# Optimization experiments

Hardware: AMD Instinct MI355X
Metric: run time of the kernel (lower is better)

## Reference

```python
import jax, jax.numpy as jnp
import numpy as np

X_DIM, Y_DIM, HIDDEN, N = 768, 768, 300, 768


def setup_inputs() -> dict:
    key = jax.random.key(0)
    ks = jax.random.split(key, 7)
    lim1 = 1.0 / np.sqrt(X_DIM + Y_DIM)
    lim2 = 1.0 / np.sqrt(HIDDEN)
    return {
        "x_samples": jax.random.normal(ks[0], (N, X_DIM), dtype=jnp.float32),
        "y_samples": jax.random.normal(ks[1], (N, Y_DIM), dtype=jnp.float32),
        "perm": jax.random.permutation(ks[2], N).astype(jnp.int32),
        # Linear 1: (x_dim+y_dim) -> hidden, torch default uniform init
        "W1": jax.random.uniform(ks[3], (HIDDEN, X_DIM + Y_DIM), jnp.float32, -lim1, lim1),
        "b1": jax.random.uniform(ks[4], (HIDDEN,), jnp.float32, -lim1, lim1),
        # Linear 2: hidden -> 1
        "W2": jax.random.uniform(ks[5], (1, HIDDEN), jnp.float32, -lim2, lim2),
        "b2": jax.random.uniform(ks[6], (1,), jnp.float32, -lim2, lim2),
    }


def reference(x_samples, y_samples, perm, W1, b1, W2, b2):
    n = x_samples.shape[0]
    x_dim = x_samples.shape[1]
    # First linear is separable across the concat: split W1 into x- and y-parts.
    hx = x_samples @ W1[:, :x_dim].T            # [N, H]
    hy = y_samples @ W1[:, x_dim:].T            # [N, H]
    w2 = W2[0]                                   # [H]
    # T0: matched pairs (x_i, y_i)
    t0 = jax.nn.softplus(jax.nn.relu(hx + hy + b1) @ w2 + b2[0])   # [N]
    # T1[i, j] = F(x_j, y_perm[i]) -- pairwise tile, [N, N, H] intermediate
    hyp = hy[perm]                               # [N, H]
    hpair = jax.nn.relu(hyp[:, None, :] + hx[None, :, :] + b1)     # [N, N, H]
    t1 = jax.nn.softplus(hpair @ w2 + b2[0])     # [N, N]
    lower_bound = t0.mean() - (jax.nn.logsumexp(t1, axis=1).mean() - jnp.log(n).astype(t1.dtype))
    return lower_bound
```

## Files before the change

kernel.cpp:

```cpp
#include <hip/hip_runtime.h>
#include <math.h>

#define NN   768
#define HH   300
#define HPAD 320
#define KD   768

#define P_OFF    0
#define PKS_STR  245760
#define PG_STR   1966080
#define CF_OFF   3932160
#define AF_OFF   4177920
#define SP_OFF   4423680
#define SP_STR   589824
#define ES_OFF   9142272
#define T0_OFF   9143040

__global__ __launch_bounds__(256) void k1_gemm(
    const float* __restrict__ x, const float* __restrict__ y,
    const int* __restrict__ perm, const float* __restrict__ W1,
    float* __restrict__ wsf)
{
    const int tid = threadIdx.x;
    const int tx = tid & 15;
    const int ty = tid >> 4;
    const int i0 = blockIdx.x * 128;
    const int h0 = blockIdx.y * 64;
    const int g  = blockIdx.z & 1;
    const int ks = blockIdx.z >> 1;
    const int kbeg = ks * 96;

    const float* src = g ? y : x;
    const int koff = g ? KD : 0;

    __shared__ float Xt[32][132];
    __shared__ float Wt[32][68];

    float4 acc[4][2];
    #pragma unroll
    for (int r = 0; r < 4; ++r) { acc[r][0] = make_float4(0,0,0,0);
                                  acc[r][1] = make_float4(0,0,0,0); }

    const int kq = (tid & 7) << 2;
    const float* xp[4];
    int xr[4];
    #pragma unroll
    for (int it = 0; it < 4; ++it) {
        int row = ((tid + it*256) >> 3);
        int gr = i0 + row;
        if (g) gr = perm[gr];
        xp[it] = src + (size_t)gr * KD + kbeg + kq;
        xr[it] = row;
    }
    const float* wp[2];
    int wr[2]; bool wv[2];
    #pragma unroll
    for (int it = 0; it < 2; ++it) {
        int hrow = ((tid + it*256) >> 3);
        int hg = h0 + hrow;
        wv[it] = hg < HH;
        wp[it] = W1 + (size_t)(wv[it] ? hg : 0) * (2*KD) + koff + kbeg + kq;
        wr[it] = hrow;
    }

    for (int kb = 0; kb < 96; kb += 32) {
        float4 xv[4], wvv[2];
        #pragma unroll
        for (int it = 0; it < 4; ++it) xv[it] = *(const float4*)(xp[it] + kb);
        #pragma unroll
        for (int it = 0; it < 2; ++it) {
            wvv[it] = *(const float4*)(wp[it] + kb);
            if (!wv[it]) wvv[it] = make_float4(0,0,0,0);
        }
        if (kb) __syncthreads();
        #pragma unroll
        for (int it = 0; it < 4; ++it) {
            Xt[kq+0][xr[it]] = xv[it].x; Xt[kq+1][xr[it]] = xv[it].y;
            Xt[kq+2][xr[it]] = xv[it].z; Xt[kq+3][xr[it]] = xv[it].w;
        }
        #pragma unroll
        for (int it = 0; it < 2; ++it) {
            Wt[kq+0][wr[it]] = wvv[it].x; Wt[kq+1][wr[it]] = wvv[it].y;
            Wt[kq+2][wr[it]] = wvv[it].z; Wt[kq+3][wr[it]] = wvv[it].w;
        }
        __syncthreads();

        #pragma unroll 8
        for (int k = 0; k < 32; ++k) {
            float4 a  = *(const float4*)&Wt[k][4*ty];
            float4 b0 = *(const float4*)&Xt[k][4*tx];
            float4 b1v = *(const float4*)&Xt[k][64 + 4*tx];
            float ar[4] = {a.x, a.y, a.z, a.w};
            #pragma unroll
            for (int r = 0; r < 4; ++r) {
                acc[r][0].x = fmaf(ar[r], b0.x,  acc[r][0].x);
                acc[r][0].y = fmaf(ar[r], b0.y,  acc[r][0].y);
                acc[r][0].z = fmaf(ar[r], b0.z,  acc[r][0].z);
                acc[r][0].w = fmaf(ar[r], b0.w,  acc[r][0].w);
                acc[r][1].x = fmaf(ar[r], b1v.x, acc[r][1].x);
                acc[r][1].y = fmaf(ar[r], b1v.y, acc[r][1].y);
                acc[r][1].z = fmaf(ar[r], b1v.z, acc[r][1].z);
                acc[r][1].w = fmaf(ar[r], b1v.w, acc[r][1].w);
            }
        }
    }

    float* dst = wsf + P_OFF + (size_t)(g*8 + ks) * PKS_STR;
    #pragma unroll
    for (int r = 0; r < 4; ++r) {
        float* rp = dst + (size_t)(h0 + 4*ty + r) * NN + i0;
        *(float4*)(rp + 4*tx)      = acc[r][0];
        *(float4*)(rp + 64 + 4*tx) = acc[r][1];
    }
}

__global__ __launch_bounds__(256) void k1b_combine(
    const float* __restrict__ b1, float* __restrict__ wsf)
{
    int idx = blockIdx.x * 256 + threadIdx.x;
    int g = idx >= 61440;
    int rem = idx - g * 61440;
    int h = rem / 192;
    int i4 = (rem % 192) * 4;

    float4 o = make_float4(0.f,0.f,0.f,0.f);
    if (h < HH) {
        const float* p = wsf + P_OFF + (size_t)g * PG_STR + (size_t)h * NN + i4;
        #pragma unroll
        for (int ks = 0; ks < 8; ++ks) {
            float4 v = *(const float4*)(p + (size_t)ks * PKS_STR);
            o.x += v.x; o.y += v.y; o.z += v.z; o.w += v.w;
        }
        if (g) {
            float bv = b1[h];
            o.x += bv; o.y += bv; o.z += bv; o.w += bv;
        }
    }
    float* dst = wsf + (g ? AF_OFF : CF_OFF) + (size_t)h * NN + i4;
    *(float4*)dst = o;
}

__global__ __launch_bounds__(256) void k2_pair(
    const float* __restrict__ wsf, const float* __restrict__ w2,
    float* __restrict__ sp)
{
    const int tid = threadIdx.x;
    const int tx = tid & 15;
    const int ty = tid >> 4;
    const int j0 = blockIdx.x * 128;
    const int i0 = blockIdx.y * 64;
    const int p  = blockIdx.z;
    const int h0 = p * 38;

    const float* AF = wsf + AF_OFF;
    const float* CF = wsf + CF_OFF;

    __shared__ float As[38][68];
    __shared__ float Cs[38][132];
    __shared__ float w2s[38];

    for (int e = tid; e < 608; e += 256) {
        int h = e >> 4, q = (e & 15) * 4;
        *(float4*)&As[h][q] = *(const float4*)(AF + (size_t)(h0 + h) * NN + i0 + q);
    }
    for (int e = tid; e < 1216; e += 256) {
        int h = e >> 5, q = (e & 31) * 4;
        *(float4*)&Cs[h][q] = *(const float4*)(CF + (size_t)(h0 + h) * NN + j0 + q);
    }
    if (tid < 38) {
        int h = h0 + tid;
        w2s[tid] = (h < HH) ? w2[h] : 0.f;
    }
    __syncthreads();

    float acc[4][8];
    #pragma unroll
    for (int r = 0; r < 4; ++r)
        #pragma unroll
        for (int c = 0; c < 8; ++c) acc[r][c] = 0.f;

    #pragma unroll 2
    for (int h = 0; h < 38; ++h) {
        float wh = w2s[h];
        float4 av = *(const float4*)&As[h][4*ty];
        float4 c0 = *(const float4*)&Cs[h][4*tx];
        float4 c1 = *(const float4*)&Cs[h][64 + 4*tx];
        float ar[4] = {av.x, av.y, av.z, av.w};
        float cr[8] = {c0.x, c0.y, c0.z, c0.w, c1.x, c1.y, c1.z, c1.w};
        #pragma unroll
        for (int r = 0; r < 4; ++r) {
            #pragma unroll
            for (int c = 0; c < 8; ++c) {
                float t = fmaxf(ar[r] + cr[c], 0.f);
                acc[r][c] = fmaf(t, wh, acc[r][c]);
            }
        }
    }

    float* dst = sp + (size_t)p * SP_STR;
    #pragma unroll
    for (int r = 0; r < 4; ++r) {
        float* rp = dst + (size_t)(i0 + 4*ty + r) * NN + j0;
        *(float4*)(rp + 4*tx) =
            make_float4(acc[r][0], acc[r][1], acc[r][2], acc[r][3]);
        *(float4*)(rp + 64 + 4*tx) =
            make_float4(acc[r][4], acc[r][5], acc[r][6], acc[r][7]);
    }
}

__global__ __launch_bounds__(256) void k2e_rows(
    const float* __restrict__ wsf, const int* __restrict__ perm,
    const float* __restrict__ b2,
    float* __restrict__ esum, float* __restrict__ t0c)
{
    const int tid = threadIdx.x;
    const float b2v = b2[0];
    const int row = blockIdx.x;
    const int pj = perm[row];
    const float* spr = wsf + SP_OFF + (size_t)row * NN;
    __shared__ float red[256];

    float e = 0.f;
    #pragma unroll
    for (int jj = 0; jj < 3; ++jj) {
        int j = tid + jj * 256;
        float s = 0.f;
        #pragma unroll
        for (int p = 0; p < 8; ++p) s += spr[(size_t)p * SP_STR + j];
        float u = s + b2v;
        e += expf(u);
        if (j == pj) {
            t0c[row] = (u > 0.f) ? u + log1pf(expf(-u)) : log1pf(expf(u));
        }
    }
    red[tid] = e;
    __syncthreads();
    for (int s = 128; s > 0; s >>= 1) {
        if (tid < s) red[tid] += red[tid + s];
        __syncthreads();
    }
    if (tid == 0) esum[row] = red[0];
}

__global__ __launch_bounds__(256) void k3_final(
    const float* __restrict__ wsf, float* __restrict__ out)
{
    const int tid = threadIdx.x;
    const float* esum = wsf + ES_OFF;
    const float* t0   = wsf + T0_OFF;

    double st0 = 0.0, slse = 0.0;
    for (int i = tid; i < NN; i += 256) {
        st0  += (double)t0[i];
        slse += log((double)NN + (double)esum[i]);
    }
    __shared__ double sa[256], sb[256];
    sa[tid] = st0; sb[tid] = slse;
    __syncthreads();
    for (int s = 128; s > 0; s >>= 1) {
        if (tid < s) { sa[tid] += sa[tid+s]; sb[tid] += sb[tid+s]; }
        __syncthreads();
    }
    if (tid == 0) {
        double lb = st0 = sa[0]/(double)NN - (sb[0]/(double)NN - log((double)NN));
        out[0] = (float)lb;
    }
}

extern "C" void kernel_launch(void* const* d_in, const int* in_sizes, int n_in,
                              void* d_out, int out_size, void* d_ws, size_t ws_size,
                              hipStream_t stream) {
    const float* x    = (const float*)d_in[0];
    const float* y    = (const float*)d_in[1];
    const int*   perm = (const int*)  d_in[2];
    const float* W1   = (const float*)d_in[3];
    const float* b1   = (const float*)d_in[4];
    const float* W2   = (const float*)d_in[5];
    const float* b2   = (const float*)d_in[6];
    float* wsf = (float*)d_ws;
    float* out = (float*)d_out;

    k1_gemm    <<<dim3(6,5,16),  256, 0, stream>>>(x, y, perm, W1, wsf);
    k1b_combine<<<480,           256, 0, stream>>>(b1, wsf);
    k2_pair    <<<dim3(6,12,8),  256, 0, stream>>>(wsf, W2, wsf + SP_OFF);
    k2e_rows   <<<NN,            256, 0, stream>>>(wsf, perm, b2,
                                                   wsf + ES_OFF, wsf + T0_OFF);
    k3_final   <<<1,             256, 0, stream>>>(wsf, out);
}
```

Baseline: 118.6 us.

## Retile pairwise kernel to 4 hidden splits and fuse final reduction via atomic counter

The pairwise relu-dot kernel is retiled to 48x96 output tiles with 75 hidden units per split and 4 splits instead of 8. This halves the partial-sum buffers written and then re-read by the row kernel, and drops the padded hidden tail. The final scalar reduction kernel is folded into the row kernel with a last-block-done atomic counter, which removes one launch. The cost is a 3x6 per-thread microtile, which does less register reuse per LDS read, plus some extra atomics and fences.

```diff
diff --git a/kernel.cpp b/kernel.cpp
--- a/kernel.cpp
+++ b/kernel.cpp
@@ -3,7 +3,6 @@
 
 #define NN   768
 #define HH   300
-#define HPAD 320
 #define KD   768
 
 #define P_OFF    0
@@ -15,6 +14,7 @@
 #define SP_STR   589824
 #define ES_OFF   9142272
 #define T0_OFF   9143040
+#define CNT_OFF  9143808
 
 __global__ __launch_bounds__(256) void k1_gemm(
     const float* __restrict__ x, const float* __restrict__ y,
@@ -118,6 +118,7 @@
     const float* __restrict__ b1, float* __restrict__ wsf)
 {
     int idx = blockIdx.x * 256 + threadIdx.x;
+    if (idx == 0) *(unsigned int*)(wsf + CNT_OFF) = 0u;
     int g = idx >= 61440;
     int rem = idx - g * 61440;
     int h = rem / 192;
@@ -147,50 +148,48 @@
     const int tid = threadIdx.x;
     const int tx = tid & 15;
     const int ty = tid >> 4;
-    const int j0 = blockIdx.x * 128;
-    const int i0 = blockIdx.y * 64;
+    const int j0 = blockIdx.x * 96;
+    const int i0 = blockIdx.y * 48;
     const int p  = blockIdx.z;
-    const int h0 = p * 38;
+    const int h0 = p * 75;
 
     const float* AF = wsf + AF_OFF;
     const float* CF = wsf + CF_OFF;
 
-    __shared__ float As[38][68];
-    __shared__ float Cs[38][132];
-    __shared__ float w2s[38];
-
-    for (int e = tid; e < 608; e += 256) {
-        int h = e >> 4, q = (e & 15) * 4;
+    __shared__ float As[75][52];
+    __shared__ float Cs[75][100];
+    __shared__ float w2s[75];
+
+    for (int e = tid; e < 900; e += 256) {
+        int h = e / 12, q = (e % 12) * 4;
         *(float4*)&As[h][q] = *(const float4*)(AF + (size_t)(h0 + h) * NN + i0 + q);
     }
-    for (int e = tid; e < 1216; e += 256) {
-        int h = e >> 5, q = (e & 31) * 4;
+    for (int e = tid; e < 1800; e += 256) {
+        int h = e / 24, q = (e % 24) * 4;
         *(float4*)&Cs[h][q] = *(const float4*)(CF + (size_t)(h0 + h) * NN + j0 + q);
     }
-    if (tid < 38) {
-        int h = h0 + tid;
-        w2s[tid] = (h < HH) ? w2[h] : 0.f;
-    }
+    if (tid < 75) w2s[tid] = w2[h0 + tid];
     __syncthreads();
 
-    float acc[4][8];
-    #pragma unroll
-    for (int r = 0; r < 4; ++r)
-        #pragma unroll
-        for (int c = 0; c < 8; ++c) acc[r][c] = 0.f;
-
-    #pragma unroll 2
-    for (int h = 0; h < 38; ++h) {
+    float acc[3][6];
+    #pragma unroll
+    for (int r = 0; r < 3; ++r)
+        #pragma unroll
+        for (int c = 0; c < 6; ++c) acc[r][c] = 0.f;
+
+    #pragma unroll 3
+    for (int h = 0; h < 75; ++h) {
         float wh = w2s[h];
-        float4 av = *(const float4*)&As[h][4*ty];
-        float4 c0 = *(const float4*)&Cs[h][4*tx];
-        float4 c1 = *(const float4*)&Cs[h][64 + 4*tx];
-        float ar[4] = {av.x, av.y, av.z, av.w};
-        float cr[8] = {c0.x, c0.y, c0.z, c0.w, c1.x, c1.y, c1.z, c1.w};
-        #pragma unroll
-        for (int r = 0; r < 4; ++r) {
+        float2 a01 = *(const float2*)&As[h][2*ty];
+        float  a2  = As[h][32 + ty];
+        float4 c03 = *(const float4*)&Cs[h][4*tx];
+        float2 c45 = *(const float2*)&Cs[h][64 + 2*tx];
+        float ar[3] = {a01.x, a01.y, a2};
+        float cr[6] = {c03.x, c03.y, c03.z, c03.w, c45.x, c45.y};
+        #pragma unroll
+        for (int r = 0; r < 3; ++r) {
             #pragma unroll
-            for (int c = 0; c < 8; ++c) {
+            for (int c = 0; c < 6; ++c) {
                 float t = fmaxf(ar[r] + cr[c], 0.f);
                 acc[r][c] = fmaf(t, wh, acc[r][c]);
             }
@@ -199,19 +198,20 @@
 
     float* dst = sp + (size_t)p * SP_STR;
     #pragma unroll
-    for (int r = 0; r < 4; ++r) {
-        float* rp = dst + (size_t)(i0 + 4*ty + r) * NN + j0;
+    for (int r = 0; r < 3; ++r) {
+        int i = (r < 2) ? (i0 + 2*ty + r) : (i0 + 32 + ty);
+        float* rp = dst + (size_t)i * NN + j0;
         *(float4*)(rp + 4*tx) =
             make_float4(acc[r][0], acc[r][1], acc[r][2], acc[r][3]);
-        *(float4*)(rp + 64 + 4*tx) =
-            make_float4(acc[r][4], acc[r][5], acc[r][6], acc[r][7]);
+        *(float2*)(rp + 64 + 2*tx) = make_float2(acc[r][4], acc[r][5]);
     }
 }
 
 __global__ __launch_bounds__(256) void k2e_rows(
     const float* __restrict__ wsf, const int* __restrict__ perm,
     const float* __restrict__ b2,
-    float* __restrict__ esum, float* __restrict__ t0c)
+    float* __restrict__ esum, float* __restrict__ t0c,
+    unsigned int* __restrict__ cnt, float* __restrict__ out)
 {
     const int tid = threadIdx.x;
     const float b2v = b2[0];
@@ -219,18 +219,21 @@
     const int pj = perm[row];
     const float* spr = wsf + SP_OFF + (size_t)row * NN;
     __shared__ float red[256];
+    __shared__ int last;
 
     float e = 0.f;
     #pragma unroll
     for (int jj = 0; jj < 3; ++jj) {
         int j = tid + jj * 256;
-        float s = 0.f;
-        #pragma unroll
-        for (int p = 0; p < 8; ++p) s += spr[(size_t)p * SP_STR + j];
+        float s = spr[j]
+                + spr[(size_t)1 * SP_STR + j]
+                + spr[(size_t)2 * SP_STR + j]
+                + spr[(size_t)3 * SP_STR + j];
         float u = s + b2v;
         e += expf(u);
         if (j == pj) {
-            t0c[row] = (u > 0.f) ? u + log1pf(expf(-u)) : log1pf(expf(u));
+            float t0 = (u > 0.f) ? u + log1pf(expf(-u)) : log1pf(expf(u));
+            atomicExch(&t0c[row], t0);
         }
     }
     red[tid] = e;
@@ -239,31 +242,34 @@
         if (tid < s) red[tid] += red[tid + s];
         __syncthreads();
     }
-    if (tid == 0) esum[row] = red[0];
-}
-
-__global__ __launch_bounds__(256) void k3_final(
-    const float* __restrict__ wsf, float* __restrict__ out)
-{
-    const int tid = threadIdx.x;
-    const float* esum = wsf + ES_OFF;
-    const float* t0   = wsf + T0_OFF;
-
-    double st0 = 0.0, slse = 0.0;
-    for (int i = tid; i < NN; i += 256) {
-        st0  += (double)t0[i];
-        slse += log((double)NN + (double)esum[i]);
-    }
-    __shared__ double sa[256], sb[256];
-    sa[tid] = st0; sb[tid] = slse;
+    if (tid == 0) {
+        atomicExch(&esum[row], red[0]);
+        __threadfence();
+        unsigned int old = atomicAdd(cnt, 1u);
+        last = (old == (unsigned int)(NN - 1));
+    }
     __syncthreads();
-    for (int s = 128; s > 0; s >>= 1) {
-        if (tid < s) { sa[tid] += sa[tid+s]; sb[tid] += sb[tid+s]; }
+
+    if (last) {
+        __threadfence();
+        double st0 = 0.0, slse = 0.0;
+        for (int i = tid; i < NN; i += 256) {
+            float es = atomicAdd(&esum[i], 0.f);
+            float t0 = atomicAdd(&t0c[i],  0.f);
+            slse += log((double)NN + (double)es);
+            st0  += (double)t0;
+        }
+        __shared__ double sa[256], sb[256];
+        sa[tid] = st0; sb[tid] = slse;
         __syncthreads();
-    }
-    if (tid == 0) {
-        double lb = st0 = sa[0]/(double)NN - (sb[0]/(double)NN - log((double)NN));
-        out[0] = (float)lb;
+        for (int s = 128; s > 0; s >>= 1) {
+            if (tid < s) { sa[tid] += sa[tid+s]; sb[tid] += sb[tid+s]; }
+            __syncthreads();
+        }
+        if (tid == 0) {
+            double lb = sa[0]/(double)NN - (sb[0]/(double)NN - log((double)NN));
+            out[0] = (float)lb;
+        }
     }
 }
 
@@ -282,8 +288,9 @@
 
     k1_gemm    <<<dim3(6,5,16),  256, 0, stream>>>(x, y, perm, W1, wsf);
     k1b_combine<<<480,           256, 0, stream>>>(b1, wsf);
-    k2_pair    <<<dim3(6,12,8),  256, 0, stream>>>(wsf, W2, wsf + SP_OFF);
+    k2_pair    <<<dim3(8,16,4),  256, 0, stream>>>(wsf, W2, wsf + SP_OFF);
     k2e_rows   <<<NN,            256, 0, stream>>>(wsf, perm, b2,
-                                                   wsf + ES_OFF, wsf + T0_OFF);
-    k3_final   <<<1,             256, 0, stream>>>(wsf, out);
-}
+                                                   wsf + ES_OFF, wsf + T0_OFF,
+                                                   (unsigned int*)(wsf + CNT_OFF),
+                                                   out);
+}
```

After: 127.2 us. 1.07x slower.
